# Kernel tuning notes

Measured on AMD Instinct MI355X. Metric: run time of the kernel, lower is better.

The kernel has to match this reference:

```python
import jax, jax.numpy as jnp
import numpy as np

B, N, D, P, K = 4, 2048, 512, 16, 4
EPS_BW = 1e-8
EPS_LN = 1e-5


def setup_inputs() -> dict:
    key = jax.random.key(0)
    ks = jax.random.split(key, 8)
    charge = jax.random.normal(ks[0], (B, N, D), dtype=jnp.float32)
    position = jax.random.normal(ks[1], (B, N, P), dtype=jnp.float32)
    mass = jax.random.uniform(ks[2], (B, N, 1), dtype=jnp.float32)
    # parameters
    log_bandwidth = jnp.zeros((K,), dtype=jnp.float32)
    W_charge = jax.random.normal(ks[3], (D * K, D), dtype=jnp.float32) / np.sqrt(D)   # torch Linear weight (out,in)
    W_combine = jax.random.normal(ks[4], (D, D * K), dtype=jnp.float32) / np.sqrt(D * K)
    gamma = jnp.ones((D,), dtype=jnp.float32)
    beta = jnp.zeros((D,), dtype=jnp.float32)
    return {"charge": charge, "position": position, "mass": mass,
            "log_bandwidth": log_bandwidth, "W_charge": W_charge,
            "W_combine": W_combine, "gamma": gamma, "beta": beta}


def reference(charge, position, mass, log_bandwidth, W_charge, W_combine, gamma, beta):
    # pairwise squared distances: (B, N, N)
    diff = position[:, :, None, :] - position[:, None, :, :]
    dist_sq = jnp.sum(diff * diff, axis=-1)
    # multi-bandwidth Gaussian kernels: (B, N, N, K)
    bandwidths = jnp.exp(log_bandwidth)
    kernels = jnp.exp(-dist_sq[..., None] / (2.0 * bandwidths + EPS_BW))
    # mass weighting: mass (B,N,1) -> (B,1,N,1), broadcast over query axis and kernels
    weighted_kernels = kernels * mass[:, None, :, :]
    # project charges: (B, N, K, D)
    projected = (charge @ W_charge.T).reshape(B, N, K, D)
    # aggregate over neighbours j: field[b,i,k,d] = sum_j wk[b,i,j,k] * proj[b,j,k,d]
    field = jnp.einsum('bijk,bjkd->bikd', weighted_kernels, projected)
    field = field.reshape(B, N, K * D) @ W_combine.T  # (B, N, D)
    # LayerNorm
    mean = jnp.mean(field, axis=-1, keepdims=True)
    var = jnp.var(field, axis=-1, keepdims=True)
    normed = (field - mean) * jax.lax.rsqrt(var + EPS_LN)
    return normed * gamma + beta
```

## Files before the change

kernel.cpp:

```cpp
#include <hip/hip_runtime.h>


typedef __bf16 bf16x8 __attribute__((ext_vector_type(8)));
typedef float f32x4 __attribute__((ext_vector_type(4)));

__device__ __forceinline__ unsigned short f2bf(float f) {
    unsigned u = __float_as_uint(f);
    unsigned r = (u + 0x7fffu + ((u >> 16) & 1u)) >> 16;
    return (unsigned short)r;
}
__device__ __forceinline__ float bf2f(unsigned short h) {
    return __uint_as_float(((unsigned)h) << 16);
}
__device__ __forceinline__ void g2l16(const unsigned short* g, unsigned short* l) {
    __builtin_amdgcn_global_load_lds(
        (const __attribute__((address_space(1))) unsigned int*)g,
        (__attribute__((address_space(3))) unsigned int*)l, 16, 0, 0);
}

__global__ __launch_bounds__(256) void k0_all(const float* __restrict__ charge,
                                              const float* __restrict__ Wc,
                                              const float* __restrict__ pos,
                                              unsigned short* __restrict__ ch16,
                                              unsigned short* __restrict__ wc16,
                                              unsigned short* __restrict__ posA,
                                              unsigned short* __restrict__ posB1,
                                              unsigned short* __restrict__ posB2,
                                              float* __restrict__ rsq)
{
    const int bx = blockIdx.x, tid = threadIdx.x;
    if (bx < 5120) {
        const float* src = (bx < 4096) ? charge : Wc;
        unsigned short* dst = (bx < 4096) ? ch16 : wc16;
        size_t i = (size_t)(bx < 4096 ? bx : bx - 4096) * 256 + tid;
        float4 v = reinterpret_cast<const float4*>(src)[i];
        unsigned short o[4] = {f2bf(v.x), f2bf(v.y), f2bf(v.z), f2bf(v.w)};
        reinterpret_cast<uint2*>(dst)[i] = *reinterpret_cast<uint2*>(&o[0]);
        return;
    }
    const int row = (bx - 5120) * 256 + tid;
    const float* src = &pos[(size_t)row * 16];
    float p[16];
#pragma unroll
    for (int cc = 0; cc < 4; cc++) {
        float4 v = *reinterpret_cast<const float4*>(&src[cc * 4]);
        p[cc * 4 + 0] = v.x; p[cc * 4 + 1] = v.y; p[cc * 4 + 2] = v.z; p[cc * 4 + 3] = v.w;
    }
    float r = 0.f;
    unsigned short h[16], lo[16], z[8] = {0, 0, 0, 0, 0, 0, 0, 0};
#pragma unroll
    for (int d = 0; d < 16; d++) {
        r = __builtin_fmaf(p[d], p[d], r);
        h[d] = f2bf(p[d]);
        lo[d] = f2bf(p[d] - bf2f(h[d]));
    }
    rsq[row] = r;
    size_t o = (size_t)row * 32;
    *reinterpret_cast<int4*>(&posA[o + 0])   = *reinterpret_cast<int4*>(&h[0]);
    *reinterpret_cast<int4*>(&posA[o + 8])   = *reinterpret_cast<int4*>(&h[8]);
    *reinterpret_cast<int4*>(&posA[o + 16])  = *reinterpret_cast<int4*>(&lo[0]);
    *reinterpret_cast<int4*>(&posA[o + 24])  = *reinterpret_cast<int4*>(&lo[8]);
    *reinterpret_cast<int4*>(&posB1[o + 0])  = *reinterpret_cast<int4*>(&h[0]);
    *reinterpret_cast<int4*>(&posB1[o + 8])  = *reinterpret_cast<int4*>(&h[8]);
    *reinterpret_cast<int4*>(&posB1[o + 16]) = *reinterpret_cast<int4*>(&h[0]);
    *reinterpret_cast<int4*>(&posB1[o + 24]) = *reinterpret_cast<int4*>(&h[8]);
    *reinterpret_cast<int4*>(&posB2[o + 0])  = *reinterpret_cast<int4*>(&lo[0]);
    *reinterpret_cast<int4*>(&posB2[o + 8])  = *reinterpret_cast<int4*>(&lo[8]);
    *reinterpret_cast<int4*>(&posB2[o + 16]) = *reinterpret_cast<int4*>(&z[0]);
    *reinterpret_cast<int4*>(&posB2[o + 24]) = *reinterpret_cast<int4*>(&z[0]);
}

__global__ __launch_bounds__(256) void k0_cvt(const float* __restrict__ src,
                                              unsigned short* __restrict__ dst)
{
    size_t i = (size_t)blockIdx.x * 256 + threadIdx.x;
    float4 v = reinterpret_cast<const float4*>(src)[i];
    unsigned short o[4] = {f2bf(v.x), f2bf(v.y), f2bf(v.z), f2bf(v.w)};
    reinterpret_cast<uint2*>(dst)[i] = *reinterpret_cast<uint2*>(&o[0]);
}

__global__ __launch_bounds__(256, 3) void k1_proj(const unsigned short* __restrict__ wc16,
                                                  const unsigned short* __restrict__ ch16,
                                                  const float* __restrict__ mass,
                                                  unsigned short* __restrict__ projm_t)
{
    __shared__ alignas(16) unsigned short As[2][128 * 32];
    __shared__ alignas(16) unsigned short Bs[2][128 * 32];
    const int tid = threadIdx.x, lane = tid & 63, wid = tid >> 6;
    const int q = lane >> 4, l15 = lane & 15;
    const int sw = (l15 >> 2) & 3;
    const int m0 = blockIdx.y * 128, n0 = blockIdx.x * 128;
    const int wm = (wid & 1) * 64, wn = (wid >> 1) * 64;

    f32x4 acc[4][4];
#pragma unroll
    for (int i = 0; i < 4; i++)
#pragma unroll
        for (int j = 0; j < 4; j++) acc[i][j] = (f32x4){0.f, 0.f, 0.f, 0.f};

#pragma unroll
    for (int q4 = 0; q4 < 4; q4++) {
        int chunk = q4 * 256 + tid;
        int ww = chunk & 511, row = ww >> 2;
        int gc4 = (ww & 3) ^ ((ww >> 4) & 3);
        if (chunk < 512)
            g2l16(&wc16[(size_t)(m0 + row) * 512 + gc4 * 8], &As[0][ww * 8]);
        else
            g2l16(&ch16[(size_t)(n0 + row) * 512 + gc4 * 8], &Bs[0][ww * 8]);
    }

    for (int n = 0; n < 16; n++) {
        const int p = n & 1;
        __syncthreads();
        const int k1 = (n + 1) * 32;
        if (k1 < 512) {
#pragma unroll
            for (int q4 = 0; q4 < 4; q4++) {
                int chunk = q4 * 256 + tid;
                int ww = chunk & 511, row = ww >> 2;
                int gc4 = (ww & 3) ^ ((ww >> 4) & 3);
                if (chunk < 512)
                    g2l16(&wc16[(size_t)(m0 + row) * 512 + k1 + gc4 * 8], &As[p ^ 1][ww * 8]);
                else
                    g2l16(&ch16[(size_t)(n0 + row) * 512 + k1 + gc4 * 8], &Bs[p ^ 1][ww * 8]);
            }
        }
        bf16x8 af[4], bfr[4];
#pragma unroll
        for (int it = 0; it < 4; it++)
            af[it] = *reinterpret_cast<const bf16x8*>(&As[p][(wm + it * 16 + l15) * 32 + (q ^ sw) * 8]);
#pragma unroll
        for (int ct = 0; ct < 4; ct++)
            bfr[ct] = *reinterpret_cast<const bf16x8*>(&Bs[p][(wn + ct * 16 + l15) * 32 + (q ^ sw) * 8]);
#pragma unroll
        for (int it = 0; it < 4; it++)
#pragma unroll
            for (int ct = 0; ct < 4; ct++)
                acc[it][ct] = __builtin_amdgcn_mfma_f32_16x16x32_bf16(af[it], bfr[ct], acc[it][ct], 0, 0, 0);
    }
#pragma unroll
    for (int ct = 0; ct < 4; ct++) {
        int nn = n0 + wn + ct * 16 + l15;
        float mf = mass[nn];
#pragma unroll
        for (int it = 0; it < 4; it++) {
            int mrow = m0 + wm + it * 16 + q * 4;
#pragma unroll
            for (int r = 0; r < 4; r++)
                projm_t[(size_t)(mrow + r) * 8192 + nn] = f2bf(acc[it][ct][r] * mf);
        }
    }
}

__global__ __launch_bounds__(256, 2) void k2_field(const unsigned short* __restrict__ posA,
                                                   const unsigned short* __restrict__ posB1,
                                                   const unsigned short* __restrict__ posB2,
                                                   const float* __restrict__ rsq,
                                                   const float* __restrict__ logbw,
                                                   const unsigned short* __restrict__ projm_t,
                                                   unsigned short* __restrict__ field)
{
    __shared__ alignas(16) unsigned short Bs[2][256 * 32];
    __shared__ alignas(16) unsigned short Wl[2][128 * 40];

    const int tid = threadIdx.x, lane = tid & 63, wid = tid >> 6;
    const int q = lane >> 4, l15 = lane & 15;
    const int sw = (l15 >> 2) & 3;
    const int L = blockIdx.x;
    const int xcd = L & 7, idx = L >> 3;
    const int i_t = idx & 15, cb = xcd * 4 + (idx >> 4);
    const int c0 = (cb & 7) * 256, b = cb >> 3;
    const int i0 = i_t * 128;
    const int kb = c0 >> 9;
    const float bw = __expf(logbw[kb]);
    const float s2 = -1.4426950408889634f / (2.0f * bw + 1e-8f);
    const float c2 = -2.0f * s2;
    const int bN = b * 2048;

    bf16x8 afG[2];
    float riS2[2][4];
#pragma unroll
    for (int t = 0; t < 2; t++) {
        afG[t] = *reinterpret_cast<const bf16x8*>(
            &posA[(size_t)(bN + i0 + wid * 32 + t * 16 + l15) * 32 + q * 8]);
#pragma unroll
        for (int r = 0; r < 4; r++)
            riS2[t][r] = rsq[bN + i0 + wid * 32 + t * 16 + q * 4 + r] * s2;
    }

    const int wo_i = (wid >> 1) * 64, wo_c = (wid & 1) * 128;
    const size_t gbase = (size_t)c0 * 8192 + bN;

    f32x4 acc[4][8];
#pragma unroll
    for (int i = 0; i < 4; i++)
#pragma unroll
        for (int j = 0; j < 8; j++) acc[i][j] = (f32x4){0.f, 0.f, 0.f, 0.f};

    bf16x8 gb1[2], gb2[2];
    float rj2[2];
#pragma unroll
    for (int jt2 = 0; jt2 < 2; jt2++) {
        int j = bN + jt2 * 16 + l15;
        gb1[jt2] = *reinterpret_cast<const bf16x8*>(&posB1[(size_t)j * 32 + q * 8]);
        gb2[jt2] = *reinterpret_cast<const bf16x8*>(&posB2[(size_t)j * 32 + q * 8]);
        rj2[jt2] = rsq[j] * s2;
    }
#pragma unroll
    for (int q4 = 0; q4 < 4; q4++) {
        int chunk = q4 * 256 + tid;
        int row = chunk >> 2, gc4 = (chunk & 3) ^ ((chunk >> 4) & 3);
        g2l16(&projm_t[gbase + (size_t)row * 8192 + gc4 * 8], &Bs[0][chunk * 8]);
    }

    for (int n = 0; n < 64; n++) {
        const int p = n & 1;
#pragma unroll
        for (int jt2 = 0; jt2 < 2; jt2++) {
#pragma unroll
            for (int t = 0; t < 2; t++) {
                f32x4 z = (f32x4){0.f, 0.f, 0.f, 0.f};
                f32x4 g1 = __builtin_amdgcn_mfma_f32_16x16x32_bf16(afG[t], gb1[jt2], z, 0, 0, 0);
                f32x4 g2 = __builtin_amdgcn_mfma_f32_16x16x32_bf16(afG[t], gb2[jt2], z, 0, 0, 0);
#pragma unroll
                for (int r = 0; r < 4; r++) {
                    float x = __builtin_fmaf(g1[r] + g2[r], c2, riS2[t][r] + rj2[jt2]);
                    Wl[p][(wid * 32 + t * 16 + q * 4 + r) * 40 + jt2 * 16 + l15] =
                        f2bf(__builtin_amdgcn_exp2f(x));
                }
            }
        }
        __syncthreads();
        if (n + 1 < 64) {
            const int j0n = (n + 1) * 32;
#pragma unroll
            for (int jt2 = 0; jt2 < 2; jt2++) {
                int j = bN + j0n + jt2 * 16 + l15;
                gb1[jt2] = *reinterpret_cast<const bf16x8*>(&posB1[(size_t)j * 32 + q * 8]);
                gb2[jt2] = *reinterpret_cast<const bf16x8*>(&posB2[(size_t)j * 32 + q * 8]);
                rj2[jt2] = rsq[j] * s2;
            }
            const size_t gb = gbase + j0n;
#pragma unroll
            for (int q4 = 0; q4 < 4; q4++) {
                int chunk = q4 * 256 + tid;
                int row = chunk >> 2, gc4 = (chunk & 3) ^ ((chunk >> 4) & 3);
                g2l16(&projm_t[gb + (size_t)row * 8192 + gc4 * 8], &Bs[p ^ 1][chunk * 8]);
            }
        }
        bf16x8 af[4], bfr[8];
#pragma unroll
        for (int it = 0; it < 4; it++)
            af[it] = *reinterpret_cast<const bf16x8*>(&Wl[p][(wo_i + it * 16 + l15) * 40 + q * 8]);
#pragma unroll
        for (int ct = 0; ct < 8; ct++)
            bfr[ct] = *reinterpret_cast<const bf16x8*>(&Bs[p][(wo_c + ct * 16 + l15) * 32 + (q ^ sw) * 8]);
#pragma unroll
        for (int it = 0; it < 4; it++)
#pragma unroll
            for (int ct = 0; ct < 8; ct++)
                acc[it][ct] = __builtin_amdgcn_mfma_f32_16x16x32_bf16(af[it], bfr[ct], acc[it][ct], 0, 0, 0);
    }
#pragma unroll
    for (int it = 0; it < 4; it++) {
#pragma unroll
        for (int ct = 0; ct < 8; ct++) {
            int gi = bN + i0 + wo_i + it * 16 + q * 4;
            int gc = c0 + wo_c + ct * 16 + l15;
#pragma unroll
            for (int r = 0; r < 4; r++)
                field[(size_t)(gi + r) * 2048 + gc] = f2bf(acc[it][ct][r]);
        }
    }
}

__global__ __launch_bounds__(256, 3) void k3_combine(const unsigned short* __restrict__ field,
                                                     const unsigned short* __restrict__ wcb16,
                                                     float* __restrict__ out)
{
    __shared__ alignas(16) unsigned short As[2][64 * 64];
    __shared__ alignas(16) unsigned short Bs[2][128 * 64];
    const int tid = threadIdx.x, lane = tid & 63, wid = tid >> 6;
    const int q = lane >> 4, l15 = lane & 15;
    const int m0 = blockIdx.y * 64, n0 = blockIdx.x * 128;
    const int wn = wid * 32;

    f32x4 acc[4][2];
#pragma unroll
    for (int i = 0; i < 4; i++)
#pragma unroll
        for (int j = 0; j < 2; j++) acc[i][j] = (f32x4){0.f, 0.f, 0.f, 0.f};

#pragma unroll
    for (int q6 = 0; q6 < 6; q6++) {
        int chunk = q6 * 256 + tid;
        if (chunk < 512) {
            int row = chunk >> 3, lc = chunk & 7;
            g2l16(&field[(size_t)(m0 + row) * 2048 + ((lc ^ (row & 7)) * 8)],
                  &As[0][chunk * 8]);
        } else {
            int w = chunk - 512, row = w >> 3, lc = w & 7;
            g2l16(&wcb16[(size_t)(n0 + row) * 2048 + ((lc ^ (row & 7)) * 8)],
                  &Bs[0][w * 8]);
        }
    }

    for (int n = 0; n < 32; n++) {
        const int p = n & 1;
        __syncthreads();
        const int k1 = (n + 1) * 64;
        if (k1 < 2048) {
#pragma unroll
            for (int q6 = 0; q6 < 6; q6++) {
                int chunk = q6 * 256 + tid;
                if (chunk < 512) {
                    int row = chunk >> 3, lc = chunk & 7;
                    g2l16(&field[(size_t)(m0 + row) * 2048 + k1 + ((lc ^ (row & 7)) * 8)],
                          &As[p ^ 1][chunk * 8]);
                } else {
                    int w = chunk - 512, row = w >> 3, lc = w & 7;
                    g2l16(&wcb16[(size_t)(n0 + row) * 2048 + k1 + ((lc ^ (row & 7)) * 8)],
                          &Bs[p ^ 1][w * 8]);
                }
            }
        }
#pragma unroll
        for (int kk = 0; kk < 2; kk++) {
            bf16x8 af[4], bfr[2];
#pragma unroll
            for (int it = 0; it < 4; it++) {
                int row = it * 16 + l15;
                af[it] = *reinterpret_cast<const bf16x8*>(
                    &As[p][row * 64 + (((kk * 4 + q) ^ (row & 7)) * 8)]);
            }
#pragma unroll
            for (int ct = 0; ct < 2; ct++) {
                int row = wn + ct * 16 + l15;
                bfr[ct] = *reinterpret_cast<const bf16x8*>(
                    &Bs[p][row * 64 + (((kk * 4 + q) ^ (row & 7)) * 8)]);
            }
#pragma unroll
            for (int it = 0; it < 4; it++)
#pragma unroll
                for (int ct = 0; ct < 2; ct++)
                    acc[it][ct] = __builtin_amdgcn_mfma_f32_16x16x32_bf16(af[it], bfr[ct], acc[it][ct], 0, 0, 0);
        }
    }
#pragma unroll
    for (int it = 0; it < 4; it++) {
#pragma unroll
        for (int ct = 0; ct < 2; ct++) {
            int m = m0 + it * 16 + q * 4;
            int nn = n0 + wn + ct * 16 + l15;
#pragma unroll
            for (int r = 0; r < 4; r++)
                out[(size_t)(m + r) * 512 + nn] = acc[it][ct][r];
        }
    }
}

__global__ __launch_bounds__(256) void k4_ln(float* __restrict__ out,
                                             const float* __restrict__ gamma,
                                             const float* __restrict__ beta)
{
    __shared__ float red[8];
    const int row = blockIdx.x, tid = threadIdx.x;
    float2 x = *reinterpret_cast<const float2*>(&out[(size_t)row * 512 + tid * 2]);
    float s = x.x + x.y;
    float ss = x.x * x.x + x.y * x.y;
#pragma unroll
    for (int off = 32; off > 0; off >>= 1) {
        s += __shfl_down(s, off);
        ss += __shfl_down(ss, off);
    }
    int wid = tid >> 6;
    if ((tid & 63) == 0) { red[wid * 2] = s; red[wid * 2 + 1] = ss; }
    __syncthreads();
    s = red[0] + red[2] + red[4] + red[6];
    ss = red[1] + red[3] + red[5] + red[7];
    float mean = s * (1.f / 512.f);
    float var = ss * (1.f / 512.f) - mean * mean;
    float inv = rsqrtf(var + 1e-5f);
    float g0 = gamma[tid * 2], g1 = gamma[tid * 2 + 1];
    float b0 = beta[tid * 2], b1 = beta[tid * 2 + 1];
    float2 o;
    o.x = (x.x - mean) * inv * g0 + b0;
    o.y = (x.y - mean) * inv * g1 + b1;
    *reinterpret_cast<float2*>(&out[(size_t)row * 512 + tid * 2]) = o;
}

extern "C" void kernel_launch(void* const* d_in, const int* in_sizes, int n_in,
                              void* d_out, int out_size, void* d_ws, size_t ws_size,
                              hipStream_t stream)
{
    const float* charge   = (const float*)d_in[0];
    const float* position = (const float*)d_in[1];
    const float* mass     = (const float*)d_in[2];
    const float* logbw    = (const float*)d_in[3];
    const float* Wc       = (const float*)d_in[4];
    const float* Wcb      = (const float*)d_in[5];
    const float* gamma    = (const float*)d_in[6];
    const float* beta     = (const float*)d_in[7];

    unsigned short* projm_t = (unsigned short*)d_ws;
    unsigned short* field   = projm_t + (size_t)2048 * 8192;
    unsigned short* wcb16   = projm_t;
    unsigned short* ch16    = field;
    unsigned short* wc16    = field + (size_t)8192 * 512;
    unsigned short* posA  = (unsigned short*)d_out;
    unsigned short* posB1 = posA + (size_t)8192 * 32;
    unsigned short* posB2 = posB1 + (size_t)8192 * 32;
    float* rsq = (float*)(posB2 + (size_t)8192 * 32);
    float* out = (float*)d_out;

    k0_all<<<5152, 256, 0, stream>>>(charge, Wc, position, ch16, wc16, posA, posB1, posB2, rsq);
    k1_proj<<<dim3(64, 16), 256, 0, stream>>>(wc16, ch16, mass, projm_t);
    k2_field<<<512, 256, 0, stream>>>(posA, posB1, posB2, rsq, logbw, projm_t, field);
    k0_cvt<<<1024, 256, 0, stream>>>(Wcb, wcb16);
    k3_combine<<<dim3(4, 128), 256, 0, stream>>>(field, wcb16, out);
    k4_ln<<<8192, 256, 0, stream>>>(out, gamma, beta);
}
```

Baseline: 271.1 us.

## Compute kernel weights directly in MFMA operand layout, drop LDS staging in field kernel

The field kernel now computes each wave's Gaussian weight tile with transposed distance MFMAs, so the results already sit in the A-operand register layout. It packs them to bf16 in registers instead of writing them to shared memory and reading them back. The projection kernel writes its output with a permuted column order so the field kernel can load B fragments straight from global memory. This removes all LDS buffers and __syncthreads from the main loop. The trade-offs are redundant exp work across waves that share rows, and uncoalesced, unpipelined global loads of the projected operand.

```diff
diff --git a/kernel.cpp b/kernel.cpp
--- a/kernel.cpp
+++ b/kernel.cpp
@@ -1,4 +1,5 @@
 #include <hip/hip_runtime.h>
+#include <hip/hip_bf16.h>
 
 
 typedef __bf16 bf16x8 __attribute__((ext_vector_type(8)));
@@ -16,6 +17,9 @@
     __builtin_amdgcn_global_load_lds(
         (const __attribute__((address_space(1))) unsigned int*)g,
         (__attribute__((address_space(3))) unsigned int*)l, 16, 0, 0);
+}
+__device__ __forceinline__ int perm32(int j32) {
+    return ((j32 & 12) << 1) | (j32 & 3) | ((j32 & 16) >> 2);
 }
 
 __global__ __launch_bounds__(256) void k0_all(const float* __restrict__ charge,
@@ -82,7 +86,7 @@
 __global__ __launch_bounds__(256, 3) void k1_proj(const unsigned short* __restrict__ wc16,
                                                   const unsigned short* __restrict__ ch16,
                                                   const float* __restrict__ mass,
-                                                  unsigned short* __restrict__ projm_t)
+                                                  unsigned short* __restrict__ projm_p)
 {
     __shared__ alignas(16) unsigned short As[2][128 * 32];
     __shared__ alignas(16) unsigned short Bs[2][128 * 32];
@@ -142,12 +146,14 @@
     for (int ct = 0; ct < 4; ct++) {
         int nn = n0 + wn + ct * 16 + l15;
         float mf = mass[nn];
+        int j32 = (ct & 1) * 16 + l15;
+        int npos = (nn - j32) | perm32(j32);
 #pragma unroll
         for (int it = 0; it < 4; it++) {
             int mrow = m0 + wm + it * 16 + q * 4;
 #pragma unroll
             for (int r = 0; r < 4; r++)
-                projm_t[(size_t)(mrow + r) * 8192 + nn] = f2bf(acc[it][ct][r] * mf);
+                projm_p[(size_t)(mrow + r) * 8192 + npos] = f2bf(acc[it][ct][r] * mf);
         }
     }
 }
@@ -157,15 +163,11 @@
                                                    const unsigned short* __restrict__ posB2,
                                                    const float* __restrict__ rsq,
                                                    const float* __restrict__ logbw,
-                                                   const unsigned short* __restrict__ projm_t,
+                                                   const unsigned short* __restrict__ projm_p,
                                                    unsigned short* __restrict__ field)
 {
-    __shared__ alignas(16) unsigned short Bs[2][256 * 32];
-    __shared__ alignas(16) unsigned short Wl[2][128 * 40];
-
     const int tid = threadIdx.x, lane = tid & 63, wid = tid >> 6;
     const int q = lane >> 4, l15 = lane & 15;
-    const int sw = (l15 >> 2) & 3;
     const int L = blockIdx.x;
     const int xcd = L & 7, idx = L >> 3;
     const int i_t = idx & 15, cb = xcd * 4 + (idx >> 4);
@@ -176,20 +178,17 @@
     const float s2 = -1.4426950408889634f / (2.0f * bw + 1e-8f);
     const float c2 = -2.0f * s2;
     const int bN = b * 2048;
-
-    bf16x8 afG[2];
-    float riS2[2][4];
-#pragma unroll
-    for (int t = 0; t < 2; t++) {
-        afG[t] = *reinterpret_cast<const bf16x8*>(
-            &posA[(size_t)(bN + i0 + wid * 32 + t * 16 + l15) * 32 + q * 8]);
-#pragma unroll
-        for (int r = 0; r < 4; r++)
-            riS2[t][r] = rsq[bN + i0 + wid * 32 + t * 16 + q * 4 + r] * s2;
-    }
-
     const int wo_i = (wid >> 1) * 64, wo_c = (wid & 1) * 128;
-    const size_t gbase = (size_t)c0 * 8192 + bN;
+
+    bf16x8 Bi1[4], Bi2[4];
+    float riS2[4];
+#pragma unroll
+    for (int it = 0; it < 4; it++) {
+        int i = bN + i0 + wo_i + it * 16 + l15;
+        Bi1[it] = *reinterpret_cast<const bf16x8*>(&posB1[(size_t)i * 32 + q * 8]);
+        Bi2[it] = *reinterpret_cast<const bf16x8*>(&posB2[(size_t)i * 32 + q * 8]);
+        riS2[it] = rsq[i] * s2;
+    }
 
     f32x4 acc[4][8];
 #pragma unroll
@@ -197,64 +196,47 @@
 #pragma unroll
         for (int j = 0; j < 8; j++) acc[i][j] = (f32x4){0.f, 0.f, 0.f, 0.f};
 
-    bf16x8 gb1[2], gb2[2];
-    float rj2[2];
-#pragma unroll
-    for (int jt2 = 0; jt2 < 2; jt2++) {
-        int j = bN + jt2 * 16 + l15;
-        gb1[jt2] = *reinterpret_cast<const bf16x8*>(&posB1[(size_t)j * 32 + q * 8]);
-        gb2[jt2] = *reinterpret_cast<const bf16x8*>(&posB2[(size_t)j * 32 + q * 8]);
-        rj2[jt2] = rsq[j] * s2;
-    }
-#pragma unroll
-    for (int q4 = 0; q4 < 4; q4++) {
-        int chunk = q4 * 256 + tid;
-        int row = chunk >> 2, gc4 = (chunk & 3) ^ ((chunk >> 4) & 3);
-        g2l16(&projm_t[gbase + (size_t)row * 8192 + gc4 * 8], &Bs[0][chunk * 8]);
-    }
+    const size_t crow = (size_t)(c0 + wo_c) * 8192 + bN;
 
     for (int n = 0; n < 64; n++) {
-        const int p = n & 1;
-#pragma unroll
-        for (int jt2 = 0; jt2 < 2; jt2++) {
-#pragma unroll
-            for (int t = 0; t < 2; t++) {
+        const int j0 = n * 32;
+        bf16x8 Aj[2];
+        f32x4 rj2[2];
+#pragma unroll
+        for (int jt = 0; jt < 2; jt++) {
+            Aj[jt] = *reinterpret_cast<const bf16x8*>(
+                &posA[(size_t)(bN + j0 + jt * 16 + l15) * 32 + q * 8]);
+            f32x4 rv = *reinterpret_cast<const f32x4*>(&rsq[bN + j0 + jt * 16 + q * 4]);
+            rj2[jt] = rv * s2;
+        }
+        bf16x8 bfr[8];
+#pragma unroll
+        for (int ct = 0; ct < 8; ct++)
+            bfr[ct] = *reinterpret_cast<const bf16x8*>(
+                &projm_p[crow + (size_t)(ct * 16 + l15) * 8192 + j0 + q * 8]);
+        bf16x8 af[4];
+#pragma unroll
+        for (int it = 0; it < 4; it++) {
+            float w8[8];
+#pragma unroll
+            for (int jt = 0; jt < 2; jt++) {
                 f32x4 z = (f32x4){0.f, 0.f, 0.f, 0.f};
-                f32x4 g1 = __builtin_amdgcn_mfma_f32_16x16x32_bf16(afG[t], gb1[jt2], z, 0, 0, 0);
-                f32x4 g2 = __builtin_amdgcn_mfma_f32_16x16x32_bf16(afG[t], gb2[jt2], z, 0, 0, 0);
+                f32x4 g = __builtin_amdgcn_mfma_f32_16x16x32_bf16(Aj[jt], Bi2[it], z, 0, 0, 0);
+                g = __builtin_amdgcn_mfma_f32_16x16x32_bf16(Aj[jt], Bi1[it], g, 0, 0, 0);
 #pragma unroll
                 for (int r = 0; r < 4; r++) {
-                    float x = __builtin_fmaf(g1[r] + g2[r], c2, riS2[t][r] + rj2[jt2]);
-                    Wl[p][(wid * 32 + t * 16 + q * 4 + r) * 40 + jt2 * 16 + l15] =
-                        f2bf(__builtin_amdgcn_exp2f(x));
+                    float x = __builtin_fmaf(g[r], c2, riS2[it] + rj2[jt][r]);
+                    w8[jt * 4 + r] = __builtin_amdgcn_exp2f(x);
                 }
             }
-        }
-        __syncthreads();
-        if (n + 1 < 64) {
-            const int j0n = (n + 1) * 32;
-#pragma unroll
-            for (int jt2 = 0; jt2 < 2; jt2++) {
-                int j = bN + j0n + jt2 * 16 + l15;
-                gb1[jt2] = *reinterpret_cast<const bf16x8*>(&posB1[(size_t)j * 32 + q * 8]);
-                gb2[jt2] = *reinterpret_cast<const bf16x8*>(&posB2[(size_t)j * 32 + q * 8]);
-                rj2[jt2] = rsq[j] * s2;
-            }
-            const size_t gb = gbase + j0n;
-#pragma unroll
-            for (int q4 = 0; q4 < 4; q4++) {
-                int chunk = q4 * 256 + tid;
-                int row = chunk >> 2, gc4 = (chunk & 3) ^ ((chunk >> 4) & 3);
-                g2l16(&projm_t[gb + (size_t)row * 8192 + gc4 * 8], &Bs[p ^ 1][chunk * 8]);
-            }
-        }
-        bf16x8 af[4], bfr[8];
-#pragma unroll
-        for (int it = 0; it < 4; it++)
-            af[it] = *reinterpret_cast<const bf16x8*>(&Wl[p][(wo_i + it * 16 + l15) * 40 + q * 8]);
-#pragma unroll
-        for (int ct = 0; ct < 8; ct++)
-            bfr[ct] = *reinterpret_cast<const bf16x8*>(&Bs[p][(wo_c + ct * 16 + l15) * 32 + (q ^ sw) * 8]);
+            union { unsigned u[4]; bf16x8 v; } pk;
+#pragma unroll
+            for (int h = 0; h < 4; h++) {
+                __hip_bfloat162 b2 = __float22bfloat162_rn(float2{w8[h * 2], w8[h * 2 + 1]});
+                pk.u[h] = *reinterpret_cast<unsigned*>(&b2);
+            }
+            af[it] = pk.v;
+        }
 #pragma unroll
         for (int it = 0; it < 4; it++)
 #pragma unroll
@@ -402,9 +384,9 @@
     const float* gamma    = (const float*)d_in[6];
     const float* beta     = (const float*)d_in[7];
 
-    unsigned short* projm_t = (unsigned short*)d_ws;
-    unsigned short* field   = projm_t + (size_t)2048 * 8192;
-    unsigned short* wcb16   = projm_t;
+    unsigned short* projm_p = (unsigned short*)d_ws;
+    unsigned short* field   = projm_p + (size_t)2048 * 8192;
+    unsigned short* wcb16   = projm_p;
     unsigned short* ch16    = field;
     unsigned short* wc16    = field + (size_t)8192 * 512;
     unsigned short* posA  = (unsigned short*)d_out;
@@ -414,8 +396,8 @@
     float* out = (float*)d_out;
 
     k0_all<<<5152, 256, 0, stream>>>(charge, Wc, position, ch16, wc16, posA, posB1, posB2, rsq);
-    k1_proj<<<dim3(64, 16), 256, 0, stream>>>(wc16, ch16, mass, projm_t);
-    k2_field<<<512, 256, 0, stream>>>(posA, posB1, posB2, rsq, logbw, projm_t, field);
+    k1_proj<<<dim3(64, 16), 256, 0, stream>>>(wc16, ch16, mass, projm_p);
+    k2_field<<<512, 256, 0, stream>>>(posA, posB1, posB2, rsq, logbw, projm_p, field);
     k0_cvt<<<1024, 256, 0, stream>>>(Wcb, wcb16);
     k3_combine<<<dim3(4, 128), 256, 0, stream>>>(field, wcb16, out);
     k4_ln<<<8192, 256, 0, stream>>>(out, gamma, beta);
```

New measurement: 308.2 us. +13.7%, slower.

## Halve field-kernel row tile to 64, single-buffer kernel weights, raise occupancy

Applied to the files above, without the earlier changes.

The field kernel now uses 64 query rows per block instead of 128, doubling the grid to 1024 blocks and cutting the per-wave accumulator from 4x8 to 4x4 tiles so launch bounds can ask for 4 blocks per SIMD. The Gaussian weight tile in LDS is single-buffered, and the two syncs per iteration are rearranged so the next projm prefetch is issued before the weights are computed. The two distance MFMAs are chained into one accumulator. The aim is more waves in flight to hide latency, at the price of reloading each projm tile from global memory twice as often and adding an extra barrier per iteration.

```diff
diff --git a/kernel.cpp b/kernel.cpp
--- a/kernel.cpp
+++ b/kernel.cpp
@@ -152,7 +152,7 @@
     }
 }
 
-__global__ __launch_bounds__(256, 2) void k2_field(const unsigned short* __restrict__ posA,
+__global__ __launch_bounds__(256, 4) void k2_field(const unsigned short* __restrict__ posA,
                                                    const unsigned short* __restrict__ posB1,
                                                    const unsigned short* __restrict__ posB2,
                                                    const float* __restrict__ rsq,
@@ -161,41 +161,37 @@
                                                    unsigned short* __restrict__ field)
 {
     __shared__ alignas(16) unsigned short Bs[2][256 * 32];
-    __shared__ alignas(16) unsigned short Wl[2][128 * 40];
+    __shared__ alignas(16) unsigned short Wl[64 * 40];
 
     const int tid = threadIdx.x, lane = tid & 63, wid = tid >> 6;
     const int q = lane >> 4, l15 = lane & 15;
     const int sw = (l15 >> 2) & 3;
     const int L = blockIdx.x;
     const int xcd = L & 7, idx = L >> 3;
-    const int i_t = idx & 15, cb = xcd * 4 + (idx >> 4);
+    const int i_t = idx & 31, cb = xcd * 4 + (idx >> 5);
     const int c0 = (cb & 7) * 256, b = cb >> 3;
-    const int i0 = i_t * 128;
+    const int i0 = i_t * 64;
     const int kb = c0 >> 9;
     const float bw = __expf(logbw[kb]);
     const float s2 = -1.4426950408889634f / (2.0f * bw + 1e-8f);
     const float c2 = -2.0f * s2;
     const int bN = b * 2048;
 
-    bf16x8 afG[2];
-    float riS2[2][4];
-#pragma unroll
-    for (int t = 0; t < 2; t++) {
-        afG[t] = *reinterpret_cast<const bf16x8*>(
-            &posA[(size_t)(bN + i0 + wid * 32 + t * 16 + l15) * 32 + q * 8]);
-#pragma unroll
-        for (int r = 0; r < 4; r++)
-            riS2[t][r] = rsq[bN + i0 + wid * 32 + t * 16 + q * 4 + r] * s2;
-    }
-
-    const int wo_i = (wid >> 1) * 64, wo_c = (wid & 1) * 128;
+    const bf16x8 afG = *reinterpret_cast<const bf16x8*>(
+        &posA[(size_t)(bN + i0 + wid * 16 + l15) * 32 + q * 8]);
+    float riS2[4];
+#pragma unroll
+    for (int r = 0; r < 4; r++)
+        riS2[r] = rsq[bN + i0 + wid * 16 + q * 4 + r] * s2;
+
+    const int wo_c = wid * 64;
     const size_t gbase = (size_t)c0 * 8192 + bN;
 
-    f32x4 acc[4][8];
+    f32x4 acc[4][4];
 #pragma unroll
     for (int i = 0; i < 4; i++)
 #pragma unroll
-        for (int j = 0; j < 8; j++) acc[i][j] = (f32x4){0.f, 0.f, 0.f, 0.f};
+        for (int j = 0; j < 4; j++) acc[i][j] = (f32x4){0.f, 0.f, 0.f, 0.f};
 
     bf16x8 gb1[2], gb2[2];
     float rj2[2];
@@ -215,22 +211,28 @@
 
     for (int n = 0; n < 64; n++) {
         const int p = n & 1;
+        __syncthreads();
+        if (n + 1 < 64) {
+            const size_t gb = gbase + (n + 1) * 32;
+#pragma unroll
+            for (int q4 = 0; q4 < 4; q4++) {
+                int chunk = q4 * 256 + tid;
+                int row = chunk >> 2, gc4 = (chunk & 3) ^ ((chunk >> 4) & 3);
+                g2l16(&projm_t[gb + (size_t)row * 8192 + gc4 * 8], &Bs[p ^ 1][chunk * 8]);
+            }
+        }
 #pragma unroll
         for (int jt2 = 0; jt2 < 2; jt2++) {
-#pragma unroll
-            for (int t = 0; t < 2; t++) {
-                f32x4 z = (f32x4){0.f, 0.f, 0.f, 0.f};
-                f32x4 g1 = __builtin_amdgcn_mfma_f32_16x16x32_bf16(afG[t], gb1[jt2], z, 0, 0, 0);
-                f32x4 g2 = __builtin_amdgcn_mfma_f32_16x16x32_bf16(afG[t], gb2[jt2], z, 0, 0, 0);
-#pragma unroll
-                for (int r = 0; r < 4; r++) {
-                    float x = __builtin_fmaf(g1[r] + g2[r], c2, riS2[t][r] + rj2[jt2]);
-                    Wl[p][(wid * 32 + t * 16 + q * 4 + r) * 40 + jt2 * 16 + l15] =
-                        f2bf(__builtin_amdgcn_exp2f(x));
-                }
-            }
-        }
-        __syncthreads();
+            f32x4 z = (f32x4){0.f, 0.f, 0.f, 0.f};
+            f32x4 g = __builtin_amdgcn_mfma_f32_16x16x32_bf16(afG, gb2[jt2], z, 0, 0, 0);
+            g = __builtin_amdgcn_mfma_f32_16x16x32_bf16(afG, gb1[jt2], g, 0, 0, 0);
+#pragma unroll
+            for (int r = 0; r < 4; r++) {
+                float x = __builtin_fmaf(g[r], c2, riS2[r] + rj2[jt2]);
+                Wl[(wid * 16 + q * 4 + r) * 40 + jt2 * 16 + l15] =
+                    f2bf(__builtin_amdgcn_exp2f(x));
+            }
+        }
         if (n + 1 < 64) {
             const int j0n = (n + 1) * 32;
 #pragma unroll
@@ -240,32 +242,26 @@
                 gb2[jt2] = *reinterpret_cast<const bf16x8*>(&posB2[(size_t)j * 32 + q * 8]);
                 rj2[jt2] = rsq[j] * s2;
             }
-            const size_t gb = gbase + j0n;
-#pragma unroll
-            for (int q4 = 0; q4 < 4; q4++) {
-                int chunk = q4 * 256 + tid;
-                int row = chunk >> 2, gc4 = (chunk & 3) ^ ((chunk >> 4) & 3);
-                g2l16(&projm_t[gb + (size_t)row * 8192 + gc4 * 8], &Bs[p ^ 1][chunk * 8]);
-            }
-        }
-        bf16x8 af[4], bfr[8];
+        }
+        __syncthreads();
+        bf16x8 af[4], bfr[4];
 #pragma unroll
         for (int it = 0; it < 4; it++)
-            af[it] = *reinterpret_cast<const bf16x8*>(&Wl[p][(wo_i + it * 16 + l15) * 40 + q * 8]);
-#pragma unroll
-        for (int ct = 0; ct < 8; ct++)
+            af[it] = *reinterpret_cast<const bf16x8*>(&Wl[(it * 16 + l15) * 40 + q * 8]);
+#pragma unroll
+        for (int ct = 0; ct < 4; ct++)
             bfr[ct] = *reinterpret_cast<const bf16x8*>(&Bs[p][(wo_c + ct * 16 + l15) * 32 + (q ^ sw) * 8]);
 #pragma unroll
         for (int it = 0; it < 4; it++)
 #pragma unroll
-            for (int ct = 0; ct < 8; ct++)
+            for (int ct = 0; ct < 4; ct++)
                 acc[it][ct] = __builtin_amdgcn_mfma_f32_16x16x32_bf16(af[it], bfr[ct], acc[it][ct], 0, 0, 0);
     }
 #pragma unroll
     for (int it = 0; it < 4; it++) {
 #pragma unroll
-        for (int ct = 0; ct < 8; ct++) {
-            int gi = bN + i0 + wo_i + it * 16 + q * 4;
+        for (int ct = 0; ct < 4; ct++) {
+            int gi = bN + i0 + it * 16 + q * 4;
             int gc = c0 + wo_c + ct * 16 + l15;
 #pragma unroll
             for (int r = 0; r < 4; r++)
@@ -415,7 +411,7 @@
 
     k0_all<<<5152, 256, 0, stream>>>(charge, Wc, position, ch16, wc16, posA, posB1, posB2, rsq);
     k1_proj<<<dim3(64, 16), 256, 0, stream>>>(wc16, ch16, mass, projm_t);
-    k2_field<<<512, 256, 0, stream>>>(posA, posB1, posB2, rsq, logbw, projm_t, field);
+    k2_field<<<1024, 256, 0, stream>>>(posA, posB1, posB2, rsq, logbw, projm_t, field);
     k0_cvt<<<1024, 256, 0, stream>>>(Wcb, wcb16);
     k3_combine<<<dim3(4, 128), 256, 0, stream>>>(field, wcb16, out);
     k4_ln<<<8192, 256, 0, stream>>>(out, gamma, beta);
```

Measured after the change: 290.3 us. 7.1% more time.
